# Kernel optimization log

Hardware: AMD Instinct MI355X
Metric: run time of the kernel (lower is better)

The kernel has to match this reference:

```python
import jax, jax.numpy as jnp
import numpy as np
from jax import lax

CH = 128
COND_CH = 80
N_LAYERS = 4
KSIZE = 3
KC = CH * CH * KSIZE * N_LAYERS  # 196608 kernel channels
BC = CH * N_LAYERS               # 512 bias channels


def _conv1d(x, w, b, padding, dilation=1):
    # x: [B, Cin, T], w: [Cout, Cin, K], b: [Cout]
    y = lax.conv_general_dilated(
        x, w, window_strides=(1,), padding=[(padding, padding)],
        rhs_dilation=(dilation,), dimension_numbers=("NCW", "OIW", "NCW"))
    return y + b[None, :, None]


def setup_inputs() -> dict:
    key = jax.random.key(0)
    ks = jax.random.split(key, 10)
    B, T_audio, T_mel = 8, 16384, 32
    scale = 0.02
    return {
        "x": jax.random.normal(ks[0], (B, CH, T_audio), jnp.float32),
        "cond": jax.random.normal(ks[1], (B, COND_CH, T_mel), jnp.float32),
        # predictor net params
        "w0": jax.random.normal(ks[2], (64, COND_CH, 5), jnp.float32) * scale,
        "b0": jnp.zeros((64,), jnp.float32),
        "w1": jax.random.normal(ks[3], (64, 64, 3), jnp.float32) * scale,
        "b1": jnp.zeros((64,), jnp.float32),
        "w2": jax.random.normal(ks[4], (KC + BC, 64, 1), jnp.float32) * scale,
        "b2": jnp.zeros((KC + BC,), jnp.float32),
        # snake activation param
        "alpha": jnp.ones((1, CH, 1), jnp.float32),
    }


def reference(x, cond, w0, b0, w1, b1, w2, b2, alpha):
    # --- kernel predictor ---
    h = jax.nn.gelu(_conv1d(cond, w0, b0, padding=2), approximate=False)
    h = jax.nn.gelu(_conv1d(h, w1, b1, padding=1), approximate=False)
    out = _conv1d(h, w2, b2, padding=0)          # [B, KC+BC, T_mel]
    kernels_flat = out[:, :KC]                    # [B, KC, T_mel]
    biases_flat = out[:, KC:]                     # [B, BC, T_mel]

    B = x.shape[0]
    k_per_layer = CH * CH * KSIZE

    def per_sample_conv(xi, ki, dilation, pad):
        # xi: [ch, T], ki: [ch, ch, ksize]
        y = lax.conv_general_dilated(
            xi[None], ki, window_strides=(1,), padding=[(pad, pad)],
            rhs_dilation=(dilation,), dimension_numbers=("NCW", "OIW", "NCW"))
        return y[0]

    for i in range(N_LAYERS):
        k_flat = kernels_flat[:, i * k_per_layer:(i + 1) * k_per_layer]
        b_flat = biases_flat[:, i * CH:(i + 1) * CH]
        dilation = 2 ** i
        pad = dilation * (KSIZE - 1) // 2
        k_mean = k_flat.mean(axis=-1).reshape(B, CH, CH, KSIZE)
        b_mean = b_flat.mean(axis=-1)             # [B, ch]
        y = jax.vmap(per_sample_conv, in_axes=(0, 0, None, None))(x, k_mean, dilation, pad)
        x = y + b_mean[:, :, None] + x            # conv(+bias) with residual

    # snake activation: x + 1/(alpha+eps) * sin(alpha*x)^2
    return x + 1.0 / (alpha + 1e-08) * jnp.sin(alpha * x) ** 2
```

## Files before the change

### kernel.cpp

```cpp
#include <hip/hip_runtime.h>
#include <math.h>

#define CHN 128
#define TT 16384
#define NBATCH 8
#define KCONST 196608
#define TILE_T 64
#define GUARD 8
#define CRANGE 96
#define ROWS 112
#define LROW 128
#define FRAG 512
#define KSN 12
#define OTILE_STRIDE (KSN * FRAG)
#define BL_STRIDE (8 * OTILE_STRIDE)

typedef __bf16 bf16x8 __attribute__((ext_vector_type(8)));
typedef float  f32x4  __attribute__((ext_vector_type(4)));
typedef unsigned short u16x8 __attribute__((ext_vector_type(8)));
typedef unsigned short u16x4 __attribute__((ext_vector_type(4)));

__device__ __forceinline__ unsigned short f2bf(float f) {
    union { float f; unsigned int u; } v; v.f = f;
    unsigned int u = v.u;
    u += 0x7fffu + ((u >> 16) & 1u);
    return (unsigned short)(u >> 16);
}
__device__ __forceinline__ float b2f(unsigned short h) {
    union { float f; unsigned int u; } v; v.u = ((unsigned int)h) << 16;
    return v.f;
}

__device__ __forceinline__ float gelu_exact(float x) {
    return 0.5f * x * (1.0f + erff(x * 0.70710678118654752f));
}

__global__ __launch_bounds__(256) void k_cond0(
    const float* __restrict__ cond, const float* __restrict__ w0,
    const float* __restrict__ b0, float* __restrict__ h0)
{
    __shared__ float cS[80 * 32];
    __shared__ float wS[8 * 80 * 5];
    __shared__ float bS[8];
    int b = blockIdx.x >> 3, g = blockIdx.x & 7;
    int tid = threadIdx.x;

    for (int idx = tid; idx < 80 * 32; idx += 256) cS[idx] = cond[b * 2560 + idx];
    for (int idx = tid; idx < 8 * 400; idx += 256) wS[idx] = w0[g * 3200 + idx];
    if (tid < 8) bS[tid] = b0[g * 8 + tid];
    __syncthreads();

    int oc = tid >> 5, t = tid & 31;
    float acc = bS[oc];
    const float* wr = wS + oc * 400;
    for (int ic = 0; ic < 80; ++ic) {
        const float* cr = cS + ic * 32;
        #pragma unroll
        for (int j = 0; j < 5; ++j) {
            int tv = t - 2 + j;
            if (tv >= 0 && tv < 32) acc += wr[ic * 5 + j] * cr[tv];
        }
    }
    h0[(b * 64 + g * 8 + oc) * 32 + t] = gelu_exact(acc);
}

__global__ __launch_bounds__(256) void k_cond1(
    const float* __restrict__ h0, const float* __restrict__ w1,
    const float* __restrict__ b1, float* __restrict__ hbar)
{
    __shared__ float hS[64 * 32];
    __shared__ float wS[8 * 64 * 3];
    __shared__ float bS[8];
    int b = blockIdx.x >> 3, g = blockIdx.x & 7;
    int tid = threadIdx.x;

    for (int idx = tid; idx < 64 * 32; idx += 256) hS[idx] = h0[b * 2048 + idx];
    for (int idx = tid; idx < 8 * 192; idx += 256) wS[idx] = w1[g * 1536 + idx];
    if (tid < 8) bS[tid] = b1[g * 8 + tid];
    __syncthreads();

    int oc = tid >> 5, t = tid & 31;
    float acc = bS[oc];
    const float* wr = wS + oc * 192;
    for (int ic = 0; ic < 64; ++ic) {
        const float* hr = hS + ic * 32;
        #pragma unroll
        for (int j = 0; j < 3; ++j) {
            int tv = t - 1 + j;
            if (tv >= 0 && tv < 32) acc += wr[ic * 3 + j] * hr[tv];
        }
    }
    float v = gelu_exact(acc);
    #pragma unroll
    for (int off = 1; off < 32; off <<= 1) v += __shfl_xor(v, off, 64);
    if (t == 0) hbar[b * 64 + g * 8 + oc] = v * (1.0f / 32.0f);
}

__global__ __launch_bounds__(256) void k_weights(
    const float* __restrict__ w2, const float* __restrict__ b2,
    const float* __restrict__ hbar,
    unsigned short* __restrict__ W, float* __restrict__ bmean)
{
    __shared__ float hS[8 * 64];
    __shared__ float buf[256 * 68];
    int tid = threadIdx.x;
    for (int idx = tid; idx < 512; idx += 256) hS[idx] = hbar[idx];

    const float4* src4 = (const float4*)(w2 + (long)blockIdx.x * 16384);
    #pragma unroll
    for (int it = 0; it < 16; ++it) {
        int f = it * 256 + tid;
        float4 v = src4[f];
        int row = f >> 4, col = f & 15;
        *(float4*)&buf[row * 68 + col * 4] = v;
    }
    __syncthreads();

    long p = (long)blockIdx.x * 256 + tid;
    const float* rowp = &buf[tid * 68];
    float acc[8];
    #pragma unroll
    for (int bb = 0; bb < 8; ++bb) acc[bb] = 0.f;
    #pragma unroll
    for (int q = 0; q < 16; ++q) {
        float4 wv = *(const float4*)&rowp[q * 4];
        #pragma unroll
        for (int bb = 0; bb < 8; ++bb) {
            const float* h = hS + bb * 64 + q * 4;
            acc[bb] += wv.x * h[0] + wv.y * h[1] + wv.z * h[2] + wv.w * h[3];
        }
    }
    float bias = b2[p];
    if (p < KCONST) {
        int i = (int)(p / 49152); int r = (int)(p % 49152);
        int o = r / 384; int m = r % 384; int c = m / 3; int tp = m % 3;
        int ks = tp * 4 + (c >> 5);
        int within = ((c >> 3) & 3) * 128 + (o & 15) * 8 + (c & 7);
        long fbase = ((long)(o >> 4) * KSN + ks) * FRAG + within;
        #pragma unroll
        for (int bb = 0; bb < 8; ++bb)
            W[(long)(bb * 4 + i) * BL_STRIDE + fbase] = f2bf(acc[bb] + bias);
    } else {
        int q = (int)(p - KCONST); int i = q >> 7, o = q & 127;
        #pragma unroll
        for (int bb = 0; bb < 8; ++bb)
            bmean[(bb * 4 + i) * 128 + o] = acc[bb] + bias;
    }
}

__global__ __launch_bounds__(512, 4) void k_fused(
    const float* __restrict__ src, float* __restrict__ dst,
    const unsigned short* __restrict__ W, const float* __restrict__ bmean,
    const float* __restrict__ alpha)
{
    __shared__ __align__(16) unsigned short xs[2][ROWS * LROW];

    int tid  = threadIdx.x;
    int lane = tid & 63;
    int wave = tid >> 6;
    int b    = blockIdx.x >> 8;
    int tile = blockIdx.x & 255;
    int T0   = tile * TILE_T;

    int nrow = lane & 15;
    int quad = lane >> 4;
    int wm   = wave & 3;
    int wn   = wave >> 2;
    int o0   = wm * 32;
    int tb   = wn * 48;

    const float* xb = src + (long)b * CHN * TT;

    if (tid < 256) {
        int gi  = tid >> 4;
        int row = (gi < 8) ? gi : gi + 96;
        u16x8 z = {0, 0, 0, 0, 0, 0, 0, 0};
        *(u16x8*)&xs[1][row * LROW + (tid & 15) * 8] = z;
    }

    {
        int cb   = wm * 32;
        int c16b = wm * 4;
        int tl   = wn * 64 + lane;
        if (tl < ROWS) {
            int tg = T0 - 24 + tl;
            bool ok = (tg >= 0) && (tg < TT);
            int sw = tl & 7;
            #pragma unroll
            for (int kb = 0; kb < 4; ++kb) {
                float v[8];
                #pragma unroll
                for (int k = 0; k < 8; ++k)
                    v[k] = ok ? xb[(long)(cb + kb * 8 + k) * TT + tg] : 0.f;
                u16x8 h;
                #pragma unroll
                for (int k = 0; k < 8; ++k) h[k] = f2bf(v[k]);
                *(u16x8*)&xs[0][tl * LROW + (((c16b + kb) ^ sw) << 3)] = h;
            }
        }
    }

    f32x4 acc[2][3];
    #pragma unroll
    for (int m = 0; m < 2; ++m) {
        int obase = o0 + m * 16 + quad * 4;
        #pragma unroll
        for (int nt = 0; nt < 3; ++nt) {
            int tg = T0 - 16 + tb + nt * 16 + nrow;
            bool ok = ((unsigned)tg < (unsigned)TT);
            #pragma unroll
            for (int r = 0; r < 4; ++r)
                acc[m][nt][r] = ok ? xb[(long)(obase + r) * TT + tg] : 0.f;
        }
    }

    __syncthreads();

    #pragma unroll 1
    for (int l = 0; l < 4; ++l) {
        const int d = 1 << l;
        const unsigned short* rd = xs[l & 1];
        unsigned short* wbuf = xs[(l + 1) & 1];
        const unsigned short* Wl =
            W + (long)(b * 4 + l) * BL_STRIDE + (long)(wm * 2) * OTILE_STRIDE
              + lane * 8;

        #pragma unroll
        for (int ks = 0; ks < 12; ++ks) {
            int roff = GUARD + tb + nrow + ((ks >> 2) - 1) * d;
            int ch   = (((ks & 3) * 4 + quad) ^ (roff & 7)) << 3;
            const unsigned short* wr = Wl + ks * FRAG;
            bf16x8 a0 = *(const bf16x8*)(wr);
            bf16x8 a1 = *(const bf16x8*)(wr + OTILE_STRIDE);
            #pragma unroll
            for (int nt = 0; nt < 3; ++nt) {
                bf16x8 bf =
                    *(const bf16x8*)&rd[(roff + nt * 16) * LROW + ch];
                acc[0][nt] = __builtin_amdgcn_mfma_f32_16x16x32_bf16(
                    a0, bf, acc[0][nt], 0, 0, 0);
                acc[1][nt] = __builtin_amdgcn_mfma_f32_16x16x32_bf16(
                    a1, bf, acc[1][nt], 0, 0, 0);
            }
        }

        {
            const float* bm = bmean + (b * 4 + l) * 128;
            #pragma unroll
            for (int m = 0; m < 2; ++m) {
                int obase = o0 + m * 16 + quad * 4;
                #pragma unroll
                for (int r = 0; r < 4; ++r) {
                    float bv = bm[obase + r];
                    #pragma unroll
                    for (int nt = 0; nt < 3; ++nt)
                        acc[m][nt][r] += bv;
                }
            }
        }

        if (l < 3) {
            #pragma unroll
            for (int m = 0; m < 2; ++m) {
                int obase = o0 + m * 16 + quad * 4;
                int ch0 = obase >> 3, sub = obase & 7;
                #pragma unroll
                for (int nt = 0; nt < 3; ++nt) {
                    int trow = GUARD + tb + nt * 16 + nrow;
                    int tg = T0 - 16 + tb + nt * 16 + nrow;
                    bool ok = ((unsigned)tg < (unsigned)TT);
                    u16x4 h;
                    #pragma unroll
                    for (int r = 0; r < 4; ++r) {
                        float v = ok ? acc[m][nt][r] : 0.f;
                        h[r] = f2bf(v);
                    }
                    *(u16x4*)&wbuf[trow * LROW +
                                   (((ch0 ^ (trow & 7)) << 3) + sub)] = h;
                }
            }
            __syncthreads();
        } else {
            #pragma unroll
            for (int m = 0; m < 2; ++m) {
                #pragma unroll
                for (int r = 0; r < 4; ++r) {
                    int o = o0 + m * 16 + quad * 4 + r;
                    float av = alpha[o];
                    float rcp = 1.0f / (av + 1e-8f);
                    long rowoff = ((long)b * CHN + o) * TT + T0;
                    #pragma unroll
                    for (int nt = 0; nt < 3; ++nt) {
                        int trel0 = tb + nt * 16 - 16;
                        if ((unsigned)trel0 < 64u) {
                            float xn = acc[m][nt][r];
                            float s = __sinf(av * xn);
                            dst[rowoff + trel0 + nrow] = xn + rcp * s * s;
                        }
                    }
                }
            }
        }
    }
}

extern "C" void kernel_launch(void* const* d_in, const int* in_sizes, int n_in,
                              void* d_out, int out_size, void* d_ws, size_t ws_size,
                              hipStream_t stream) {
    const float* x     = (const float*)d_in[0];
    const float* cond  = (const float*)d_in[1];
    const float* w0    = (const float*)d_in[2];
    const float* b0    = (const float*)d_in[3];
    const float* w1    = (const float*)d_in[4];
    const float* b1    = (const float*)d_in[5];
    const float* w2    = (const float*)d_in[6];
    const float* b2    = (const float*)d_in[7];
    const float* alpha = (const float*)d_in[8];
    float* out = (float*)d_out;

    char* ws = (char*)d_ws;
    unsigned short* W = (unsigned short*)ws;
    float* bmean = (float*)(ws + 3145728);
    float* hbar  = (float*)(ws + 3162112);
    float* h0    = (float*)(ws + 3164160);

    k_cond0<<<64, 256, 0, stream>>>(cond, w0, b0, h0);
    k_cond1<<<64, 256, 0, stream>>>(h0, w1, b1, hbar);
    k_weights<<<772, 256, 0, stream>>>(w2, b2, hbar, W, bmean);
    k_fused<<<2048, 512, 0, stream>>>(x, out, W, bmean, alpha);
}
```

Before: 298.9 us.

## Widen time tile to 96 and single-buffer LDS with extra barrier

Raises the output tile from 64 to 96 time steps (128 computed columns per block, 4 n-tiles per wave) so the 16-column halo on each side is a smaller share of the work, cutting redundant MFMA and global loads. Launches a 2D grid of 171 tiles per batch. LDS drops from double to single buffer, and a barrier is added before each layer writes back into the same buffer. Risks include more accumulator registers, one extra sync per layer, and a partial last tile that needs a bounds check.

```diff
diff --git a/kernel.cpp b/kernel.cpp
--- a/kernel.cpp
+++ b/kernel.cpp
@@ -5,15 +5,16 @@
 #define TT 16384
 #define NBATCH 8
 #define KCONST 196608
-#define TILE_T 64
+#define TILE_T 96
 #define GUARD 8
-#define CRANGE 96
-#define ROWS 112
+#define CRANGE 128
+#define ROWS 144
 #define LROW 128
 #define FRAG 512
 #define KSN 12
 #define OTILE_STRIDE (KSN * FRAG)
 #define BL_STRIDE (8 * OTILE_STRIDE)
+#define NTILES 171
 
 typedef __bf16 bf16x8 __attribute__((ext_vector_type(8)));
 typedef float  f32x4  __attribute__((ext_vector_type(4)));
@@ -153,36 +154,28 @@
     const unsigned short* __restrict__ W, const float* __restrict__ bmean,
     const float* __restrict__ alpha)
 {
-    __shared__ __align__(16) unsigned short xs[2][ROWS * LROW];
+    __shared__ __align__(16) unsigned short xs[ROWS * LROW];
 
     int tid  = threadIdx.x;
     int lane = tid & 63;
     int wave = tid >> 6;
-    int b    = blockIdx.x >> 8;
-    int tile = blockIdx.x & 255;
-    int T0   = tile * TILE_T;
+    int b    = blockIdx.y;
+    int T0   = blockIdx.x * TILE_T;
 
     int nrow = lane & 15;
     int quad = lane >> 4;
     int wm   = wave & 3;
     int wn   = wave >> 2;
     int o0   = wm * 32;
-    int tb   = wn * 48;
+    int tb   = wn * 64;
 
     const float* xb = src + (long)b * CHN * TT;
-
-    if (tid < 256) {
-        int gi  = tid >> 4;
-        int row = (gi < 8) ? gi : gi + 96;
-        u16x8 z = {0, 0, 0, 0, 0, 0, 0, 0};
-        *(u16x8*)&xs[1][row * LROW + (tid & 15) * 8] = z;
-    }
 
     {
         int cb   = wm * 32;
         int c16b = wm * 4;
-        int tl   = wn * 64 + lane;
-        if (tl < ROWS) {
+        {
+            int tl = wn * 64 + lane;
             int tg = T0 - 24 + tl;
             bool ok = (tg >= 0) && (tg < TT);
             int sw = tl & 7;
@@ -195,17 +188,34 @@
                 u16x8 h;
                 #pragma unroll
                 for (int k = 0; k < 8; ++k) h[k] = f2bf(v[k]);
-                *(u16x8*)&xs[0][tl * LROW + (((c16b + kb) ^ sw) << 3)] = h;
-            }
-        }
-    }
-
-    f32x4 acc[2][3];
+                *(u16x8*)&xs[tl * LROW + (((c16b + kb) ^ sw) << 3)] = h;
+            }
+        }
+        if (wn == 0 && lane < 16) {
+            int tl = 128 + lane;
+            int tg = T0 - 24 + tl;
+            bool ok = (tg >= 0) && (tg < TT);
+            int sw = tl & 7;
+            #pragma unroll
+            for (int kb = 0; kb < 4; ++kb) {
+                float v[8];
+                #pragma unroll
+                for (int k = 0; k < 8; ++k)
+                    v[k] = ok ? xb[(long)(cb + kb * 8 + k) * TT + tg] : 0.f;
+                u16x8 h;
+                #pragma unroll
+                for (int k = 0; k < 8; ++k) h[k] = f2bf(v[k]);
+                *(u16x8*)&xs[tl * LROW + (((c16b + kb) ^ sw) << 3)] = h;
+            }
+        }
+    }
+
+    f32x4 acc[2][4];
     #pragma unroll
     for (int m = 0; m < 2; ++m) {
         int obase = o0 + m * 16 + quad * 4;
         #pragma unroll
-        for (int nt = 0; nt < 3; ++nt) {
+        for (int nt = 0; nt < 4; ++nt) {
             int tg = T0 - 16 + tb + nt * 16 + nrow;
             bool ok = ((unsigned)tg < (unsigned)TT);
             #pragma unroll
@@ -219,8 +229,6 @@
     #pragma unroll 1
     for (int l = 0; l < 4; ++l) {
         const int d = 1 << l;
-        const unsigned short* rd = xs[l & 1];
-        unsigned short* wbuf = xs[(l + 1) & 1];
         const unsigned short* Wl =
             W + (long)(b * 4 + l) * BL_STRIDE + (long)(wm * 2) * OTILE_STRIDE
               + lane * 8;
@@ -233,9 +241,9 @@
             bf16x8 a0 = *(const bf16x8*)(wr);
             bf16x8 a1 = *(const bf16x8*)(wr + OTILE_STRIDE);
             #pragma unroll
-            for (int nt = 0; nt < 3; ++nt) {
+            for (int nt = 0; nt < 4; ++nt) {
                 bf16x8 bf =
-                    *(const bf16x8*)&rd[(roff + nt * 16) * LROW + ch];
+                    *(const bf16x8*)&xs[(roff + nt * 16) * LROW + ch];
                 acc[0][nt] = __builtin_amdgcn_mfma_f32_16x16x32_bf16(
                     a0, bf, acc[0][nt], 0, 0, 0);
                 acc[1][nt] = __builtin_amdgcn_mfma_f32_16x16x32_bf16(
@@ -252,11 +260,13 @@
                 for (int r = 0; r < 4; ++r) {
                     float bv = bm[obase + r];
                     #pragma unroll
-                    for (int nt = 0; nt < 3; ++nt)
+                    for (int nt = 0; nt < 4; ++nt)
                         acc[m][nt][r] += bv;
                 }
             }
         }
+
+        __syncthreads();
 
         if (l < 3) {
             #pragma unroll
@@ -264,7 +274,7 @@
                 int obase = o0 + m * 16 + quad * 4;
                 int ch0 = obase >> 3, sub = obase & 7;
                 #pragma unroll
-                for (int nt = 0; nt < 3; ++nt) {
+                for (int nt = 0; nt < 4; ++nt) {
                     int trow = GUARD + tb + nt * 16 + nrow;
                     int tg = T0 - 16 + tb + nt * 16 + nrow;
                     bool ok = ((unsigned)tg < (unsigned)TT);
@@ -274,8 +284,8 @@
                         float v = ok ? acc[m][nt][r] : 0.f;
                         h[r] = f2bf(v);
                     }
-                    *(u16x4*)&wbuf[trow * LROW +
-                                   (((ch0 ^ (trow & 7)) << 3) + sub)] = h;
+                    *(u16x4*)&xs[trow * LROW +
+                                 (((ch0 ^ (trow & 7)) << 3) + sub)] = h;
                 }
             }
             __syncthreads();
@@ -289,12 +299,16 @@
                     float rcp = 1.0f / (av + 1e-8f);
                     long rowoff = ((long)b * CHN + o) * TT + T0;
                     #pragma unroll
-                    for (int nt = 0; nt < 3; ++nt) {
+                    for (int nt = 0; nt < 4; ++nt) {
                         int trel0 = tb + nt * 16 - 16;
-                        if ((unsigned)trel0 < 64u) {
-                            float xn = acc[m][nt][r];
-                            float s = __sinf(av * xn);
-                            dst[rowoff + trel0 + nrow] = xn + rcp * s * s;
+                        if ((unsigned)trel0 < 96u) {
+                            int tg = T0 + trel0 + nrow;
+                            if (tg < TT) {
+                                float xn = acc[m][nt][r];
+                                float s = __sinf(av * xn);
+                                dst[rowoff + trel0 + nrow] =
+                                    xn + rcp * s * s;
+                            }
                         }
                     }
                 }
@@ -326,5 +340,5 @@
     k_cond0<<<64, 256, 0, stream>>>(cond, w0, b0, h0);
     k_cond1<<<64, 256, 0, stream>>>(h0, w1, b1, hbar);
     k_weights<<<772, 256, 0, stream>>>(w2, b2, hbar, W, bmean);
-    k_fused<<<2048, 512, 0, stream>>>(x, out, W, bmean, alpha);
-}
+    k_fused<<<dim3(NTILES, NBATCH), 512, 0, stream>>>(x, out, W, bmean, alpha);
+}
```

Measured after the change: 299.1 us. About the same (+0.1%).
